# Kernel tuning notes

Measured on AMD Instinct MI355X. Metric: run time of the kernel, lower is better.

The kernel has to match this reference:

```python
import jax, jax.numpy as jnp
import numpy as np

HEADS = 8
KV_HEADS = 4
HEAD_DIM = 256
HIDDEN = 2560
WINDOW = 1024          # sliding_window (layer is sliding: (0+1) % 6 != 0)
SCALE = 256.0 ** -0.5  # query_pre_attn_scalar ** -0.5
ROPE_BASE = 10000.0    # rope_local_base_freq for sliding layers
EPS = 1e-6
NEG = -1e30


def rms_norm(x, w, eps=EPS):
    # x: [..., D]; effective weight is (1 + param) per the RMSNorm module
    var = jnp.mean(x * x, axis=-1, keepdims=True)
    return x * jax.lax.rsqrt(var + eps) * w


def rope(x, base, offset):
    # x: [B, H, T, D]; rotate-half RoPE over the full head_dim
    T, D = x.shape[2], x.shape[3]
    half = D // 2
    pos = (offset + jnp.arange(T)).astype(jnp.float32)           # [T]
    inv_freq = base ** (-jnp.arange(half, dtype=jnp.float32) * 2.0 / D)  # [half]
    ang = pos[:, None] * inv_freq[None, :]                       # [T, half]
    cos, sin = jnp.cos(ang), jnp.sin(ang)
    x1, x2 = x[..., :half], x[..., half:]
    return jnp.concatenate([x1 * cos - x2 * sin, x2 * cos + x1 * sin], axis=-1)


def setup_inputs() -> dict:
    key = jax.random.key(0)
    ks = jax.random.split(key, 7)
    B, T, S = 2, 1024, 4096
    w_std = 0.02
    return {
        "x": jax.random.normal(ks[0], (B, T, HIDDEN), dtype=jnp.float32),
        "k_cache": jax.random.normal(ks[1], (B, KV_HEADS, S, HEAD_DIM), dtype=jnp.float32),
        "v_cache": jax.random.normal(ks[2], (B, KV_HEADS, S, HEAD_DIM), dtype=jnp.float32),
        "wq": jax.random.normal(ks[3], (HIDDEN, HEADS * HEAD_DIM), dtype=jnp.float32) * w_std,
        "wk": jax.random.normal(ks[4], (HIDDEN, KV_HEADS * HEAD_DIM), dtype=jnp.float32) * w_std,
        "wv": jax.random.normal(ks[5], (HIDDEN, KV_HEADS * HEAD_DIM), dtype=jnp.float32) * w_std,
        "wo": jax.random.normal(ks[6], (HEADS * HEAD_DIM, HIDDEN), dtype=jnp.float32) * w_std,
        "q_norm_w": jnp.zeros((HEAD_DIM,), dtype=jnp.float32),
        "k_norm_w": jnp.zeros((HEAD_DIM,), dtype=jnp.float32),
        "pos_offset": 2048,
        "cache_index": 2048,
    }


def reference(x, k_cache, v_cache, wq, wk, wv, wo, q_norm_w, k_norm_w, pos_offset, cache_index):
    B, T, _ = x.shape
    # QKV projections -> [B, H, T, D]
    q = (x @ wq).reshape(B, T, HEADS, HEAD_DIM).transpose(0, 2, 1, 3)
    k = (x @ wk).reshape(B, T, KV_HEADS, HEAD_DIM).transpose(0, 2, 1, 3)
    v = (x @ wv).reshape(B, T, KV_HEADS, HEAD_DIM).transpose(0, 2, 1, 3)
    # per-head RMSNorm (effective weight 1 + param)
    q = rms_norm(q, 1.0 + q_norm_w)
    k = rms_norm(k, 1.0 + k_norm_w)
    # RoPE with position offset
    q = rope(q, ROPE_BASE, pos_offset)
    k = rope(k, ROPE_BASE, pos_offset)
    # KV cache update at cache_index along the sequence axis
    k_new = jax.lax.dynamic_update_slice(k_cache, k, (0, 0, cache_index, 0))
    v_new = jax.lax.dynamic_update_slice(v_cache, v, (0, 0, cache_index, 0))
    S = k_new.shape[2]
    # sliding-window validity mask over cached keys (as in the module: shared over queries)
    idx = jnp.arange(S)
    valid = (idx < cache_index + T) & (idx >= cache_index + T - WINDOW)   # [S]
    # GQA attention: group queries over kv heads
    G = HEADS // KV_HEADS
    qg = q.reshape(B, KV_HEADS, G, T, HEAD_DIM)
    scores = jnp.einsum('bkgtd,bksd->bkgts', qg, k_new) * SCALE           # [B,KV,G,T,S]
    scores = jnp.where(valid[None, None, None, None, :], scores, NEG)
    p = jax.nn.softmax(scores, axis=-1)
    out = jnp.einsum('bkgts,bksd->bkgtd', p, v_new)                       # [B,KV,G,T,D]
    out = out.reshape(B, HEADS, T, HEAD_DIM).transpose(0, 2, 1, 3).reshape(B, T, HEADS * HEAD_DIM)
    return out @ wo, k_new, v_new
```

## Files before the change

### kernel.cpp

```cpp
#include <hip/hip_runtime.h>

typedef __bf16 bf16;
typedef __bf16 bf16x8 __attribute__((ext_vector_type(8)));
typedef __bf16 bf16x4 __attribute__((ext_vector_type(4)));
typedef float f32x4 __attribute__((ext_vector_type(4)));

#define MFMA16(a, b, c) __builtin_amdgcn_mfma_f32_16x16x32_bf16(a, b, c, 0, 0, 0)

#define GLL(lds, g)                                                    \
  __builtin_amdgcn_global_load_lds(                                    \
      (const __attribute__((address_space(1))) void*)(g),              \
      (__attribute__((address_space(3))) void*)(lds), 16, 0, 0)

__global__ __launch_bounds__(256) void prep_kernel(
    const float* __restrict__ kc, const float* __restrict__ vc,
    float* __restrict__ kout, float* __restrict__ vout,
    const int* __restrict__ p_ci, const float* __restrict__ x,
    bf16* __restrict__ xb, const float* __restrict__ wq,
    const float* __restrict__ wk, const float* __restrict__ wv,
    bf16* __restrict__ wqkv_t, const float* __restrict__ wo,
    bf16* __restrict__ wo_t) {
  const int blk = blockIdx.x;
  const int tid = threadIdx.x;
  if (blk < 8192) {
    const int s = (blk & 1023) * 4 + (tid >> 6);
    const int bk = blk >> 10;
    const int ci = *p_ci;
    if ((unsigned)(s - ci) < 1024u) return;
    const long base = ((long)bk * 4096 + s) * 64 + (tid & 63);
    ((float4*)kout)[base] = ((const float4*)kc)[base];
    ((float4*)vout)[base] = ((const float4*)vc)[base];
    return;
  }
  if (blk < 13312) {
    const long i = (long)(blk - 8192) * 256 + tid;
    const float4 v = ((const float4*)x)[i];
    bf16x4 o4;
    o4.x = (bf16)v.x; o4.y = (bf16)v.y; o4.z = (bf16)v.z; o4.w = (bf16)v.w;
    ((bf16x4*)xb)[i] = o4;
    return;
  }
  __shared__ float tile[64][65];
  const float* src;
  int k0, n0, col, srcN, dstK;
  bf16* dst;
  if (blk < 15872) {
    const int idx = blk - 13312;
    k0 = (idx % 40) * 64; n0 = (idx / 40) * 64;
    dstK = 2560; dst = wqkv_t;
    if (n0 < 2048)      { src = wq; col = n0;        srcN = 2048; }
    else if (n0 < 3072) { src = wk; col = n0 - 2048; srcN = 1024; }
    else                { src = wv; col = n0 - 3072; srcN = 1024; }
  } else {
    const int idx = blk - 15872;
    k0 = (idx & 31) * 64; n0 = (idx >> 5) * 64;
    dstK = 2048; dst = wo_t; src = wo; col = n0; srcN = 2560;
  }
  {
    const int rf = tid >> 4, c4 = (tid & 15) * 4;
#pragma unroll
    for (int i = 0; i < 4; ++i) {
      const int r = i * 16 + rf;
      const float4 v = *(const float4*)(src + (long)(k0 + r) * srcN + col + c4);
      tile[r][c4] = v.x; tile[r][c4 + 1] = v.y;
      tile[r][c4 + 2] = v.z; tile[r][c4 + 3] = v.w;
    }
  }
  __syncthreads();
  {
    const int nf = tid >> 3, kc = (tid & 7) * 8;
#pragma unroll
    for (int i = 0; i < 2; ++i) {
      const int nn = i * 32 + nf;
      bf16x8 o8;
#pragma unroll
      for (int j = 0; j < 8; ++j) o8[j] = (bf16)tile[kc + j][nn];
      *(bf16x8*)(dst + (long)(n0 + nn) * dstK + k0 + kc) = o8;
    }
  }
}

__global__ __launch_bounds__(256) void v_trans_kernel(const bf16* __restrict__ qkv,
                                                      const int* __restrict__ p_ci,
                                                      float* __restrict__ vout,
                                                      bf16* __restrict__ vt) {
  __shared__ float tile[32][33];
  const int s0 = blockIdx.x * 32, d0 = blockIdx.y * 32, bk = blockIdx.z;
  const int b = bk >> 2, kvh = bk & 3;
  const int ci = *p_ci;
  const int tx = threadIdx.x, ty = threadIdx.y;
#pragma unroll
  for (int i = 0; i < 4; ++i) {
    const int s = s0 + ty + i * 8;
    const float val =
        (float)qkv[(long)(b * 1024 + s) * 4096 + (12 + kvh) * 256 + d0 + tx];
    tile[ty + i * 8][tx] = val;
    vout[((long)bk * 4096 + ci + s) * 256 + d0 + tx] = val;
  }
  __syncthreads();
  bf16* dstb = vt + ((long)bk * 256 + d0) * 1024 + s0;
#pragma unroll
  for (int i = 0; i < 4; ++i)
    dstb[(long)(ty + i * 8) * 1024 + tx] = (bf16)tile[tx][ty + i * 8];
}

template <int BM, int BN, int K, int N, typename OutT>
__global__ __launch_bounds__(256) void gemm_kernel(const bf16* __restrict__ A,
                                                   const bf16* __restrict__ BT,
                                                   OutT* __restrict__ C) {
  __shared__ bf16 As[2 * BM * 32];
  __shared__ bf16 Bs[2 * BN * 32];
  const int bm = blockIdx.x, bn = blockIdx.y;
  const int tid = threadIdx.x;
  const int wave = tid >> 6, lane = tid & 63;
  const int quad = lane >> 4, l16 = lane & 15;
  constexpr int WM = BM / 2, WN = BN / 2;
  constexpr int MI = WM / 16, NI = WN / 16;
  const int wm = (wave & 1) * WM, wn = (wave >> 1) * WN;
  f32x4 acc[MI][NI] = {};
  const int srow = tid >> 2;
  const int sslot = tid & 3;
  const bf16* Ag = A + (long)(bm * BM) * K;
  const bf16* Bg = BT + (long)(bn * BN) * K;
  auto stage = [&](int buf, int k0) {
#pragma unroll
    for (int i = 0; i < BM / 64; ++i) {
      const int r = i * 64 + srow;
      const int cc = (sslot - (r >> 1)) & 3;
      GLL(As + buf * BM * 32 + (i * 256 + wave * 64) * 8,
          Ag + (long)r * K + k0 + cc * 8);
    }
#pragma unroll
    for (int i = 0; i < BN / 64; ++i) {
      const int r = i * 64 + srow;
      const int cc = (sslot - (r >> 1)) & 3;
      GLL(Bs + buf * BN * 32 + (i * 256 + wave * 64) * 8,
          Bg + (long)r * K + k0 + cc * 8);
    }
  };
  stage(0, 0);
  int buf = 0;
  for (int k0 = 0; k0 < K; k0 += 32) {
    __syncthreads();
    if (k0 + 32 < K) stage(buf ^ 1, k0 + 32);
    const bf16* Ab = As + buf * BM * 32;
    const bf16* Bb = Bs + buf * BN * 32;
    bf16x8 af[MI], bfr[NI];
#pragma unroll
    for (int mi = 0; mi < MI; ++mi) {
      const int r = wm + mi * 16 + l16;
      af[mi] = *(const bf16x8*)(Ab + r * 32 + (((quad + (r >> 1)) & 3) * 8));
    }
#pragma unroll
    for (int ni = 0; ni < NI; ++ni) {
      const int r = wn + ni * 16 + l16;
      bfr[ni] = *(const bf16x8*)(Bb + r * 32 + (((quad + (r >> 1)) & 3) * 8));
    }
#pragma unroll
    for (int mi = 0; mi < MI; ++mi)
#pragma unroll
      for (int ni = 0; ni < NI; ++ni)
        acc[mi][ni] = MFMA16(af[mi], bfr[ni], acc[mi][ni]);
    buf ^= 1;
  }
  const int crow = bm * BM + wm + quad * 4;
  const int ccol = bn * BN + wn + l16;
#pragma unroll
  for (int mi = 0; mi < MI; ++mi)
#pragma unroll
    for (int ni = 0; ni < NI; ++ni)
#pragma unroll
      for (int r = 0; r < 4; ++r)
        C[(long)(crow + mi * 16 + r) * N + ccol + ni * 16] = (OutT)acc[mi][ni][r];
}

__global__ __launch_bounds__(256) void normrope_kernel(
    const bf16* __restrict__ qkv, const float* __restrict__ qw,
    const float* __restrict__ kw, const int* __restrict__ p_pos,
    const int* __restrict__ p_ci, float* __restrict__ kout,
    bf16* __restrict__ q_bf, bf16* __restrict__ k_bf) {
  const int bt = blockIdx.x, slot = blockIdx.y;
  const int t = bt & 1023, b = bt >> 10;
  const int d = threadIdx.x;
  const float val = (float)qkv[(long)bt * 4096 + slot * 256 + d];
  __shared__ float red[4];
  __shared__ float rowbuf[256];
  float ss = val * val;
#pragma unroll
  for (int i = 1; i < 64; i <<= 1) ss += __shfl_xor(ss, i);
  if ((d & 63) == 0) red[d >> 6] = ss;
  __syncthreads();
  const float tot = red[0] + red[1] + red[2] + red[3];
  const float rstd = rsqrtf(tot * (1.0f / 256.0f) + 1e-6f);
  const bool isq = slot < 8;
  const float wv = isq ? qw[d] : kw[d];
  const float nv = val * rstd * (1.0f + wv);
  rowbuf[d] = nv;
  __syncthreads();
  const int e = d & 127;
  const float inv_freq = exp2f((float)e * -0.10381025296522976f);
  const float ang = (float)(*p_pos + t) * inv_freq;
  float rev = ang * 0.15915494309189535f;
  rev = rev - floorf(rev);
  const float sn = __builtin_amdgcn_sinf(rev);
  const float cs = __builtin_amdgcn_cosf(rev);
  float outv;
  if (d < 128) outv = nv * cs - rowbuf[d + 128] * sn;
  else         outv = nv * cs + rowbuf[d - 128] * sn;
  if (isq) {
    q_bf[((long)(b * 8 + slot) * 1024 + t) * 256 + d] = (bf16)outv;
  } else {
    const int kh = slot - 8;
    const int ci = *p_ci;
    kout[((long)(b * 4 + kh) * 4096 + ci + t) * 256 + d] = outv;
    k_bf[((long)(b * 4 + kh) * 1024 + t) * 256 + d] = (bf16)outv;
  }
}

__global__ __launch_bounds__(256) void attn_kernel(const bf16* __restrict__ q_bf,
                                                   const bf16* __restrict__ k_bf,
                                                   const bf16* __restrict__ vt_bf,
                                                   bf16* __restrict__ attn) {
  __shared__ bf16 Ks[64 * 256];
  __shared__ bf16 Vs[256 * 64];
  __shared__ bf16 Ps[64 * 72];
  const int qt = blockIdx.x, h = blockIdx.y, b = blockIdx.z;
  const int kvh = h >> 1;
  const int tid = threadIdx.x;
  const int wave = tid >> 6, lane = tid & 63, quad = lane >> 4, l16 = lane & 15;
  bf16x8 qf[8];
  const bf16* qg =
      q_bf + ((long)(b * 8 + h) * 1024 + qt * 64 + wave * 16 + l16) * 256 + quad * 8;
#pragma unroll
  for (int i = 0; i < 8; ++i) qf[i] = *(const bf16x8*)(qg + i * 32);
  f32x4 o[16] = {};
  float m_r[4] = {-1e30f, -1e30f, -1e30f, -1e30f};
  float l_r[4] = {0.f, 0.f, 0.f, 0.f};
  const float sfac = 0.0625f * 1.44269504088896f;
  const bf16* kgb = k_bf + (long)(b * 4 + kvh) * 1024 * 256;
  const bf16* vgb = vt_bf + (long)(b * 4 + kvh) * 256 * 1024;
  const int krow = tid >> 5, kccp = tid & 31;
  const int kcc = kccp ^ (krow & 7);
  const int vrow0 = tid >> 3, vccp = tid & 7;
  for (int st = 0; st < 16; ++st) {
    __syncthreads();
#pragma unroll
    for (int i = 0; i < 8; ++i) {
      GLL(Ks + (i * 256 + wave * 64) * 8,
          kgb + (long)(st * 64 + krow + i * 8) * 256 + kcc * 8);
    }
#pragma unroll
    for (int i = 0; i < 8; ++i) {
      const int vr = vrow0 + i * 32;
      GLL(Vs + (i * 256 + wave * 64) * 8,
          vgb + (long)vr * 1024 + st * 64 + (vccp ^ (vr & 7)) * 8);
    }
    __syncthreads();
    f32x4 sacc[4] = {};
#pragma unroll
    for (int kk = 0; kk < 8; ++kk) {
#pragma unroll
      for (int ni = 0; ni < 4; ++ni) {
        const int r = ni * 16 + l16;
        bf16x8 kf = *(const bf16x8*)(Ks + r * 256 + (((kk * 4 + quad) ^ (r & 7)) * 8));
        sacc[ni] = MFMA16(qf[kk], kf, sacc[ni]);
      }
    }
    float alpha_r[4];
#pragma unroll
    for (int r = 0; r < 4; ++r) {
      float s0 = sacc[0][r] * sfac, s1 = sacc[1][r] * sfac;
      float s2 = sacc[2][r] * sfac, s3 = sacc[3][r] * sfac;
      float mx = fmaxf(fmaxf(s0, s1), fmaxf(s2, s3));
#pragma unroll
      for (int dd = 1; dd < 16; dd <<= 1) mx = fmaxf(mx, __shfl_xor(mx, dd));
      float mnew = fmaxf(m_r[r], mx);
      float al = exp2f(m_r[r] - mnew);
      m_r[r] = mnew;
      alpha_r[r] = al;
      float p0 = exp2f(s0 - mnew), p1 = exp2f(s1 - mnew);
      float p2 = exp2f(s2 - mnew), p3 = exp2f(s3 - mnew);
      float rs = p0 + p1 + p2 + p3;
#pragma unroll
      for (int dd = 1; dd < 16; dd <<= 1) rs += __shfl_xor(rs, dd);
      l_r[r] = l_r[r] * al + rs;
      const int prow = (wave * 16 + quad * 4 + r) * 72;
      Ps[prow + l16] = (bf16)p0;
      Ps[prow + 16 + l16] = (bf16)p1;
      Ps[prow + 32 + l16] = (bf16)p2;
      Ps[prow + 48 + l16] = (bf16)p3;
    }
#pragma unroll
    for (int n2 = 0; n2 < 16; ++n2) {
      f32x4 tv = o[n2];
      tv.x *= alpha_r[0]; tv.y *= alpha_r[1]; tv.z *= alpha_r[2]; tv.w *= alpha_r[3];
      o[n2] = tv;
    }
    __syncthreads();
    bf16x8 pf0 = *(const bf16x8*)(Ps + (wave * 16 + l16) * 72 + quad * 8);
    bf16x8 pf1 = *(const bf16x8*)(Ps + (wave * 16 + l16) * 72 + 32 + quad * 8);
#pragma unroll
    for (int n2 = 0; n2 < 16; ++n2) {
      const int r = n2 * 16 + l16;
      bf16x8 vf0 = *(const bf16x8*)(Vs + r * 64 + ((quad ^ (r & 7)) * 8));
      o[n2] = MFMA16(pf0, vf0, o[n2]);
      bf16x8 vf1 = *(const bf16x8*)(Vs + r * 64 + (((4 + quad) ^ (r & 7)) * 8));
      o[n2] = MFMA16(pf1, vf1, o[n2]);
    }
  }
  float inv_l[4];
#pragma unroll
  for (int r = 0; r < 4; ++r) inv_l[r] = 1.0f / l_r[r];
  bf16* og = attn + ((long)(b * 1024 + qt * 64 + wave * 16 + quad * 4)) * 2048 +
             h * 256 + l16;
#pragma unroll
  for (int n2 = 0; n2 < 16; ++n2)
#pragma unroll
    for (int r = 0; r < 4; ++r)
      og[(long)r * 2048 + n2 * 16] = (bf16)(o[n2][r] * inv_l[r]);
}

extern "C" void kernel_launch(void* const* d_in, const int* in_sizes, int n_in,
                              void* d_out, int out_size, void* d_ws, size_t ws_size,
                              hipStream_t stream) {
  const float* x = (const float*)d_in[0];
  const float* k_cache = (const float*)d_in[1];
  const float* v_cache = (const float*)d_in[2];
  const float* wq = (const float*)d_in[3];
  const float* wk = (const float*)d_in[4];
  const float* wv = (const float*)d_in[5];
  const float* wo = (const float*)d_in[6];
  const float* qnw = (const float*)d_in[7];
  const float* knw = (const float*)d_in[8];
  const int* p_pos = (const int*)d_in[9];
  const int* p_ci = (const int*)d_in[10];

  float* out0 = (float*)d_out;
  float* kout = out0 + (long)2 * 1024 * 2560;
  float* vout = kout + (long)2 * 4 * 4096 * 256;

  char* w = (char*)d_ws;
  bf16* x_bf = (bf16*)(w);
  bf16* wqkv_t = (bf16*)(w + 10485760);
  bf16* wo_t = (bf16*)(w + 31457280);
  bf16* qkv = (bf16*)(w + 41943040);
  bf16* q_bf = (bf16*)(w + 58720256);
  bf16* k_bf = (bf16*)(w + 67108864);
  bf16* vt_bf = (bf16*)(w + 71303168);
  bf16* attn_b = (bf16*)(w + 75497472);

  prep_kernel<<<17152, 256, 0, stream>>>(k_cache, v_cache, kout, vout, p_ci, x,
                                         x_bf, wq, wk, wv, wqkv_t, wo, wo_t);

  gemm_kernel<128, 128, 2560, 4096, bf16>
      <<<dim3(16, 32), 256, 0, stream>>>(x_bf, wqkv_t, qkv);

  dim3 tb(32, 8);
  v_trans_kernel<<<dim3(32, 8, 8), tb, 0, stream>>>(qkv, p_ci, vout, vt_bf);

  normrope_kernel<<<dim3(2048, 12), 256, 0, stream>>>(qkv, qnw, knw, p_pos, p_ci,
                                                      kout, q_bf, k_bf);

  attn_kernel<<<dim3(16, 8, 2), 256, 0, stream>>>(q_bf, k_bf, vt_bf, attn_b);

  gemm_kernel<64, 128, 2048, 2560, float>
      <<<dim3(32, 20), 256, 0, stream>>>(attn_b, wo_t, out0);
}
```

Measured before the change: 396.0 us.

## Vectorize norm-RoPE per token, reorder prep work, and drop a redundant attention barrier

The norm+RoPE kernel now uses one 384-thread block per token to handle all 12 Q/K head slots. Each half-wave normalizes one 256-wide row, 8 elements per lane with vector loads and stores. The rotate-half partner now comes from a cross-lane shuffle instead of shared memory and block barriers. The prep kernel schedules the weight transposes first and gives each cast and cache-copy block more work, cutting the grid roughly in half. In attention, a __syncthreads between writing and reading the P tile is removed because each wave only reads the rows it wrote itself; this relies on intra-wave LDS ordering.

Result: no change. 401.5 us (+1.4%).

```diff
diff --git a/kernel.cpp b/kernel.cpp
--- a/kernel.cpp
+++ b/kernel.cpp
@@ -22,37 +22,46 @@
     bf16* __restrict__ wo_t) {
   const int blk = blockIdx.x;
   const int tid = threadIdx.x;
-  if (blk < 8192) {
-    const int s = (blk & 1023) * 4 + (tid >> 6);
-    const int bk = blk >> 10;
+  if (blk >= 3840) {
+    if (blk < 6400) {
+      const long i = (long)(blk - 3840) * 512 + tid;
+      const float4 v0 = ((const float4*)x)[i];
+      const float4 v1 = ((const float4*)x)[i + 256];
+      bf16x4 o0, o1;
+      o0.x = (bf16)v0.x; o0.y = (bf16)v0.y; o0.z = (bf16)v0.z; o0.w = (bf16)v0.w;
+      o1.x = (bf16)v1.x; o1.y = (bf16)v1.y; o1.z = (bf16)v1.z; o1.w = (bf16)v1.w;
+      ((bf16x4*)xb)[i] = o0;
+      ((bf16x4*)xb)[i + 256] = o1;
+      return;
+    }
+    const int cb = blk - 6400;
+    const int bk = cb >> 8;
+    const int s0 = (cb & 255) * 16 + (tid >> 6) * 4;
+    const int l = tid & 63;
     const int ci = *p_ci;
-    if ((unsigned)(s - ci) < 1024u) return;
-    const long base = ((long)bk * 4096 + s) * 64 + (tid & 63);
-    ((float4*)kout)[base] = ((const float4*)kc)[base];
-    ((float4*)vout)[base] = ((const float4*)vc)[base];
-    return;
-  }
-  if (blk < 13312) {
-    const long i = (long)(blk - 8192) * 256 + tid;
-    const float4 v = ((const float4*)x)[i];
-    bf16x4 o4;
-    o4.x = (bf16)v.x; o4.y = (bf16)v.y; o4.z = (bf16)v.z; o4.w = (bf16)v.w;
-    ((bf16x4*)xb)[i] = o4;
+#pragma unroll
+    for (int i = 0; i < 4; ++i) {
+      const int s = s0 + i;
+      if ((unsigned)(s - ci) < 1024u) continue;
+      const long base = ((long)bk * 4096 + s) * 64 + l;
+      ((float4*)kout)[base] = ((const float4*)kc)[base];
+      ((float4*)vout)[base] = ((const float4*)vc)[base];
+    }
     return;
   }
   __shared__ float tile[64][65];
   const float* src;
   int k0, n0, col, srcN, dstK;
   bf16* dst;
-  if (blk < 15872) {
-    const int idx = blk - 13312;
+  if (blk < 2560) {
+    const int idx = blk;
     k0 = (idx % 40) * 64; n0 = (idx / 40) * 64;
     dstK = 2560; dst = wqkv_t;
     if (n0 < 2048)      { src = wq; col = n0;        srcN = 2048; }
     else if (n0 < 3072) { src = wk; col = n0 - 2048; srcN = 1024; }
     else                { src = wv; col = n0 - 3072; srcN = 1024; }
   } else {
-    const int idx = blk - 15872;
+    const int idx = blk - 2560;
     k0 = (idx & 31) * 64; n0 = (idx >> 5) * 64;
     dstK = 2048; dst = wo_t; src = wo; col = n0; srcN = 2560;
   }
@@ -68,14 +77,14 @@
   }
   __syncthreads();
   {
-    const int nf = tid >> 3, kc = (tid & 7) * 8;
+    const int nf = tid >> 3, kcq = (tid & 7) * 8;
 #pragma unroll
     for (int i = 0; i < 2; ++i) {
       const int nn = i * 32 + nf;
       bf16x8 o8;
 #pragma unroll
-      for (int j = 0; j < 8; ++j) o8[j] = (bf16)tile[kc + j][nn];
-      *(bf16x8*)(dst + (long)(n0 + nn) * dstK + k0 + kc) = o8;
+      for (int j = 0; j < 8; ++j) o8[j] = (bf16)tile[kcq + j][nn];
+      *(bf16x8*)(dst + (long)(n0 + nn) * dstK + k0 + kcq) = o8;
     }
   }
 }
@@ -174,46 +183,68 @@
         C[(long)(crow + mi * 16 + r) * N + ccol + ni * 16] = (OutT)acc[mi][ni][r];
 }
 
-__global__ __launch_bounds__(256) void normrope_kernel(
+__global__ __launch_bounds__(384) void normrope_kernel(
     const bf16* __restrict__ qkv, const float* __restrict__ qw,
     const float* __restrict__ kw, const int* __restrict__ p_pos,
     const int* __restrict__ p_ci, float* __restrict__ kout,
     bf16* __restrict__ q_bf, bf16* __restrict__ k_bf) {
-  const int bt = blockIdx.x, slot = blockIdx.y;
+  const int bt = blockIdx.x;
   const int t = bt & 1023, b = bt >> 10;
-  const int d = threadIdx.x;
-  const float val = (float)qkv[(long)bt * 4096 + slot * 256 + d];
-  __shared__ float red[4];
-  __shared__ float rowbuf[256];
-  float ss = val * val;
-#pragma unroll
-  for (int i = 1; i < 64; i <<= 1) ss += __shfl_xor(ss, i);
-  if ((d & 63) == 0) red[d >> 6] = ss;
-  __syncthreads();
-  const float tot = red[0] + red[1] + red[2] + red[3];
-  const float rstd = rsqrtf(tot * (1.0f / 256.0f) + 1e-6f);
+  const int wave = threadIdx.x >> 6;
+  const int lane = threadIdx.x & 63;
+  const int half = lane >> 5;
+  const int l32 = lane & 31;
+  const int slot = wave * 2 + half;
+  const int d0 = l32 * 8;
+  const bf16x8 v8 = *(const bf16x8*)(qkv + (long)bt * 4096 + slot * 256 + d0);
+  float v[8], ss = 0.0f;
+#pragma unroll
+  for (int j = 0; j < 8; ++j) {
+    v[j] = (float)v8[j];
+    ss += v[j] * v[j];
+  }
+#pragma unroll
+  for (int i = 1; i < 32; i <<= 1) ss += __shfl_xor(ss, i);
+  const float rstd = rsqrtf(ss * (1.0f / 256.0f) + 1e-6f);
   const bool isq = slot < 8;
-  const float wv = isq ? qw[d] : kw[d];
-  const float nv = val * rstd * (1.0f + wv);
-  rowbuf[d] = nv;
-  __syncthreads();
-  const int e = d & 127;
-  const float inv_freq = exp2f((float)e * -0.10381025296522976f);
-  const float ang = (float)(*p_pos + t) * inv_freq;
-  float rev = ang * 0.15915494309189535f;
-  rev = rev - floorf(rev);
-  const float sn = __builtin_amdgcn_sinf(rev);
-  const float cs = __builtin_amdgcn_cosf(rev);
-  float outv;
-  if (d < 128) outv = nv * cs - rowbuf[d + 128] * sn;
-  else         outv = nv * cs + rowbuf[d - 128] * sn;
+  const float* wp = isq ? qw : kw;
+  const float4 w0 = *(const float4*)(wp + d0);
+  const float4 w1 = *(const float4*)(wp + d0 + 4);
+  float nv[8];
+  nv[0] = v[0] * rstd * (1.0f + w0.x); nv[1] = v[1] * rstd * (1.0f + w0.y);
+  nv[2] = v[2] * rstd * (1.0f + w0.z); nv[3] = v[3] * rstd * (1.0f + w0.w);
+  nv[4] = v[4] * rstd * (1.0f + w1.x); nv[5] = v[5] * rstd * (1.0f + w1.y);
+  nv[6] = v[6] * rstd * (1.0f + w1.z); nv[7] = v[7] * rstd * (1.0f + w1.w);
+  float pv[8];
+#pragma unroll
+  for (int j = 0; j < 8; ++j) pv[j] = __shfl_xor(nv[j], 16);
+  const float pt = (float)(*p_pos + t);
+  const int e0 = (l32 & 15) * 8;
+  float outv[8];
+#pragma unroll
+  for (int j = 0; j < 8; ++j) {
+    const float inv_freq = exp2f((float)(e0 + j) * -0.10381025296522976f);
+    float rev = pt * inv_freq * 0.15915494309189535f;
+    rev = rev - floorf(rev);
+    const float sn = __builtin_amdgcn_sinf(rev);
+    const float cs = __builtin_amdgcn_cosf(rev);
+    outv[j] = (d0 < 128) ? nv[j] * cs - pv[j] * sn : nv[j] * cs + pv[j] * sn;
+  }
+  bf16x8 ob;
+#pragma unroll
+  for (int j = 0; j < 8; ++j) ob[j] = (bf16)outv[j];
   if (isq) {
-    q_bf[((long)(b * 8 + slot) * 1024 + t) * 256 + d] = (bf16)outv;
+    *(bf16x8*)(q_bf + ((long)(b * 8 + slot) * 1024 + t) * 256 + d0) = ob;
   } else {
     const int kh = slot - 8;
     const int ci = *p_ci;
-    kout[((long)(b * 4 + kh) * 4096 + ci + t) * 256 + d] = outv;
-    k_bf[((long)(b * 4 + kh) * 1024 + t) * 256 + d] = (bf16)outv;
+    *(bf16x8*)(k_bf + ((long)(b * 4 + kh) * 1024 + t) * 256 + d0) = ob;
+    float4 f0, f1;
+    f0.x = outv[0]; f0.y = outv[1]; f0.z = outv[2]; f0.w = outv[3];
+    f1.x = outv[4]; f1.y = outv[5]; f1.z = outv[6]; f1.w = outv[7];
+    float* kg = kout + ((long)(b * 4 + kh) * 4096 + ci + t) * 256 + d0;
+    *(float4*)(kg) = f0;
+    *(float4*)(kg + 4) = f1;
   }
 }
 
@@ -296,7 +327,6 @@
       tv.x *= alpha_r[0]; tv.y *= alpha_r[1]; tv.z *= alpha_r[2]; tv.w *= alpha_r[3];
       o[n2] = tv;
     }
-    __syncthreads();
     bf16x8 pf0 = *(const bf16x8*)(Ps + (wave * 16 + l16) * 72 + quad * 8);
     bf16x8 pf1 = *(const bf16x8*)(Ps + (wave * 16 + l16) * 72 + 32 + quad * 8);
 #pragma unroll
@@ -349,8 +379,8 @@
   bf16* vt_bf = (bf16*)(w + 71303168);
   bf16* attn_b = (bf16*)(w + 75497472);
 
-  prep_kernel<<<17152, 256, 0, stream>>>(k_cache, v_cache, kout, vout, p_ci, x,
-                                         x_bf, wq, wk, wv, wqkv_t, wo, wo_t);
+  prep_kernel<<<8448, 256, 0, stream>>>(k_cache, v_cache, kout, vout, p_ci, x,
+                                        x_bf, wq, wk, wv, wqkv_t, wo, wo_t);
 
   gemm_kernel<128, 128, 2560, 4096, bf16>
       <<<dim3(16, 32), 256, 0, stream>>>(x_bf, wqkv_t, qkv);
@@ -358,8 +388,8 @@
   dim3 tb(32, 8);
   v_trans_kernel<<<dim3(32, 8, 8), tb, 0, stream>>>(qkv, p_ci, vout, vt_bf);
 
-  normrope_kernel<<<dim3(2048, 12), 256, 0, stream>>>(qkv, qnw, knw, p_pos, p_ci,
-                                                      kout, q_bf, k_bf);
+  normrope_kernel<<<2048, 384, 0, stream>>>(qkv, qnw, knw, p_pos, p_ci,
+                                            kout, q_bf, k_bf);
 
   attn_kernel<<<dim3(16, 8, 2), 256, 0, stream>>>(q_bf, k_bf, vt_bf, attn_b);
 
```
